# Optimization experiments

Measured on AMD Instinct MI355X. Metric: run time of the kernel, lower is better.

Reference implementation:

```python
import jax, jax.numpy as jnp
import numpy as np

D_MODEL = 1024
N_HEADS = 16
D_HEAD = 64


def setup_inputs() -> dict:
    key = jax.random.key(0)
    ks = jax.random.split(key, 9)
    B, T = 2, 2048
    s_in = 1.0 / np.sqrt(D_MODEL)
    s_o = 1.0 / np.sqrt(N_HEADS * D_HEAD)
    return {
        "x": jax.random.normal(ks[0], (B, T, D_MODEL), dtype=jnp.float32),
        "wq": jax.random.normal(ks[1], (D_MODEL, N_HEADS * D_HEAD), dtype=jnp.float32) * s_in,
        "bq": jax.random.normal(ks[2], (N_HEADS * D_HEAD,), dtype=jnp.float32) * 0.01,
        "wk": jax.random.normal(ks[3], (D_MODEL, N_HEADS * D_HEAD), dtype=jnp.float32) * s_in,
        "bk": jax.random.normal(ks[4], (N_HEADS * D_HEAD,), dtype=jnp.float32) * 0.01,
        "wv": jax.random.normal(ks[5], (D_MODEL, N_HEADS * D_HEAD), dtype=jnp.float32) * s_in,
        "bv": jax.random.normal(ks[6], (N_HEADS * D_HEAD,), dtype=jnp.float32) * 0.01,
        "wo": jax.random.normal(ks[7], (N_HEADS * D_HEAD, D_MODEL), dtype=jnp.float32) * s_o,
        "bo": jax.random.normal(ks[8], (D_MODEL,), dtype=jnp.float32) * 0.01,
    }


def reference(x, wq, bq, wk, bk, wv, bv, wo, bo):
    B, T, _ = x.shape
    H, Dh = N_HEADS, D_HEAD
    # projections -> [B, H, T, Dh]
    q = (x @ wq + bq).reshape(B, T, H, Dh).transpose(0, 2, 1, 3)
    k = (x @ wk + bk).reshape(B, T, H, Dh).transpose(0, 2, 1, 3)
    v = (x @ wv + bv).reshape(B, T, H, Dh).transpose(0, 2, 1, 3)
    scale = 1.0 / np.sqrt(Dh).astype(np.float32)
    attn = jnp.einsum("bhqd,bhkd->bhqk", q, k) * scale  # [B,H,T,T]
    causal = jnp.tril(jnp.ones((T, T), dtype=bool))
    attn = jnp.where(causal, attn, jnp.float32(-jnp.inf))
    attn = jax.nn.softmax(attn, axis=-1)
    out = jnp.einsum("bhqk,bhkd->bhqd", attn, v)  # [B,H,T,Dh]
    out = out.transpose(0, 2, 1, 3).reshape(B, T, H * Dh)
    return out @ wo + bo
```

## Files before the change

### kernel.cpp

```cpp
#include <hip/hip_runtime.h>
#include <math.h>

#define D_MODEL 1024
#define N_HEADS 16
#define D_HEAD  64
#define B_SZ    2
#define T_SEQ   2048

typedef short bf16x8 __attribute__((ext_vector_type(8)));
typedef short bf16x4 __attribute__((ext_vector_type(4)));
typedef float f32x4  __attribute__((ext_vector_type(4)));
typedef unsigned short us4 __attribute__((ext_vector_type(4)));

__device__ __forceinline__ unsigned short f2bf(float f) {
  union { float f; unsigned u; } v; v.f = f;
  unsigned r = v.u + 0x7FFFu + ((v.u >> 16) & 1u);
  return (unsigned short)(r >> 16);
}
__device__ __forceinline__ float bf2f(unsigned short s) {
  union { unsigned u; float f; } v; v.u = ((unsigned)s) << 16;
  return v.f;
}
__device__ __forceinline__ unsigned pack2_rtz(float lo, float hi) {
  union { float f; unsigned u; } a, b; a.f = hi; b.f = lo;
  return __builtin_amdgcn_perm(a.u, b.u, 0x07060302u);
}

__device__ __forceinline__ void async_copy16(const unsigned short* g, unsigned short* l) {
  __builtin_amdgcn_global_load_lds(
      (__attribute__((address_space(1))) void*)(g),
      (__attribute__((address_space(3))) void*)(l), 16, 0, 0);
}

__global__ __launch_bounds__(256) void conv_all(
    const float* __restrict__ x,
    const float* __restrict__ wq, const float* __restrict__ wk,
    const float* __restrict__ wv, const float* __restrict__ wo,
    unsigned short* __restrict__ wt, unsigned short* __restrict__ xb)
{
  const int z = blockIdx.z;
  if (z < 4) {
    const float* W = (z == 0) ? wq : (z == 1) ? wk : (z == 2) ? wv : wo;
    unsigned short* O = wt + (size_t)z * D_MODEL * D_MODEL;
    __shared__ float t[32][33];
    const int tx = threadIdx.x & 31, ty = threadIdx.x >> 5;
    const int kb = blockIdx.x * 32, nb = blockIdx.y * 32;
    #pragma unroll
    for (int i = 0; i < 4; i++)
      t[ty + i * 8][tx] = W[(size_t)(kb + ty + i * 8) * D_MODEL + nb + tx];
    __syncthreads();
    #pragma unroll
    for (int i = 0; i < 4; i++)
      O[(size_t)(nb + ty + i * 8) * D_MODEL + kb + tx] = f2bf(t[tx][ty + i * 8]);
  } else {
    const int row = (z - 4) * 1024 + blockIdx.y * 32 + (threadIdx.x >> 3);
    const int col = blockIdx.x * 32 + (threadIdx.x & 7) * 4;
    float4 v = *(const float4*)&x[(size_t)row * D_MODEL + col];
    us4 o = { f2bf(v.x), f2bf(v.y), f2bf(v.z), f2bf(v.w) };
    *(us4*)&xb[(size_t)row * D_MODEL + col] = o;
  }
}

#define BKg 64

__global__ __launch_bounds__(256) void qkv_gemm(
    const unsigned short* __restrict__ A, const unsigned short* __restrict__ Bt,
    const float* __restrict__ bq, const float* __restrict__ bk,
    const float* __restrict__ bv, unsigned short* __restrict__ qkv,
    unsigned short* __restrict__ vT)
{
  __shared__ unsigned short As[128 * BKg];
  __shared__ unsigned short Bs[64 * BKg];

  const int tid  = threadIdx.x;
  const int wv   = tid >> 6;
  const int lane = tid & 63;
  const int lr   = lane & 15;
  const int quad = lane >> 4;
  const int wm   = wv >> 1;
  const int wn   = wv & 1;
  const int row0 = blockIdx.x * 128;
  const int col0 = blockIdx.y * 64;
  const int K = D_MODEL;

  const int mid = col0 >> 10;
  const float* bias = (mid == 0) ? bq : (mid == 1) ? bk : bv;

  f32x4 acc[8];
  #pragma unroll
  for (int i = 0; i < 8; i++) acc[i] = (f32x4){0.f, 0.f, 0.f, 0.f};

  for (int k0 = 0; k0 < K; k0 += BKg) {
    #pragma unroll
    for (int it = 0; it < 4; it++) {
      const int gg = wv * 256 + it * 64 + lane;
      const int r  = gg >> 3;
      const int gc = ((gg & 7) ^ (r & 7)) * 8;
      async_copy16(A + (size_t)(row0 + r) * K + k0 + gc,
                   (unsigned short*)As + (size_t)(wv * 256 + it * 64) * 8);
    }
    #pragma unroll
    for (int it = 0; it < 2; it++) {
      const int gg = wv * 128 + it * 64 + lane;
      const int r  = gg >> 3;
      const int gc = ((gg & 7) ^ (r & 7)) * 8;
      async_copy16(Bt + (size_t)(col0 + r) * K + k0 + gc,
                   (unsigned short*)Bs + (size_t)(wv * 128 + it * 64) * 8);
    }
    __syncthreads();

    if (mid == 2) {
      bf16x8 aF[4][2], bF[2][2];
      #pragma unroll
      for (int hf = 0; hf < 2; hf++) {
        const int kc = (hf * 4 + quad) ^ (lr & 7);
        #pragma unroll
        for (int mi = 0; mi < 4; mi++)
          aF[mi][hf] = *(const bf16x8*)&As[(wm * 64 + mi * 16 + lr) * BKg + kc * 8];
        #pragma unroll
        for (int ni = 0; ni < 2; ni++)
          bF[ni][hf] = *(const bf16x8*)&Bs[(wn * 32 + ni * 16 + lr) * BKg + kc * 8];
      }
      #pragma unroll
      for (int hf = 0; hf < 2; hf++)
        #pragma unroll
        for (int mi = 0; mi < 4; mi++)
          #pragma unroll
          for (int ni = 0; ni < 2; ni++)
            acc[mi * 2 + ni] = __builtin_amdgcn_mfma_f32_16x16x32_bf16(
                aF[mi][hf], bF[ni][hf], acc[mi * 2 + ni], 0, 0, 0);
    } else {
      bf16x8 aF[2][2], bF[4][2];
      #pragma unroll
      for (int hf = 0; hf < 2; hf++) {
        const int kc = (hf * 4 + quad) ^ (lr & 7);
        #pragma unroll
        for (int mi = 0; mi < 2; mi++)
          aF[mi][hf] = *(const bf16x8*)&Bs[(wm * 32 + mi * 16 + lr) * BKg + kc * 8];
        #pragma unroll
        for (int ni = 0; ni < 4; ni++)
          bF[ni][hf] = *(const bf16x8*)&As[(wn * 64 + ni * 16 + lr) * BKg + kc * 8];
      }
      #pragma unroll
      for (int hf = 0; hf < 2; hf++)
        #pragma unroll
        for (int mi = 0; mi < 2; mi++)
          #pragma unroll
          for (int ni = 0; ni < 4; ni++)
            acc[mi * 4 + ni] = __builtin_amdgcn_mfma_f32_16x16x32_bf16(
                aF[mi][hf], bF[ni][hf], acc[mi * 4 + ni], 0, 0, 0);
    }
    __syncthreads();
  }

  if (mid == 2) {
    #pragma unroll
    for (int ni = 0; ni < 2; ni++) {
      const int nn = (col0 & 1023) + wn * 32 + ni * 16 + lr;
      const float bv_ = bias[nn];
      const int h = nn >> 6, d = nn & 63;
      #pragma unroll
      for (int mi = 0; mi < 4; mi++) {
        const int t0_ = row0 + wm * 64 + mi * 16 + quad * 4;
        const int b = t0_ >> 11, tl = t0_ & 2047;
        us4 o;
        #pragma unroll
        for (int i = 0; i < 4; i++) o[i] = f2bf(acc[mi * 2 + ni][i] + bv_);
        *(us4*)&vT[((size_t)(b * N_HEADS + h) * D_HEAD + d) * T_SEQ + tl] = o;
      }
    }
  } else {
    unsigned short* dst = qkv + (size_t)mid * (4096u * 1024u);
    #pragma unroll
    for (int ni = 0; ni < 4; ni++) {
      const int t = row0 + wn * 64 + ni * 16 + lr;
      const int b = t >> 11, tl = t & 2047;
      #pragma unroll
      for (int mi = 0; mi < 2; mi++) {
        const int f = (col0 & 1023) + wm * 32 + mi * 16 + quad * 4;
        const int h = f >> 6, d = f & 63;
        const float4 b4 = *(const float4*)&bias[f];
        us4 o;
        o[0] = f2bf(acc[mi * 4 + ni][0] + b4.x);
        o[1] = f2bf(acc[mi * 4 + ni][1] + b4.y);
        o[2] = f2bf(acc[mi * 4 + ni][2] + b4.z);
        o[3] = f2bf(acc[mi * 4 + ni][3] + b4.w);
        *(us4*)&dst[((size_t)(b * N_HEADS + h) * T_SEQ + tl) * D_HEAD + d] = o;
      }
    }
  }
}

__global__ __launch_bounds__(256) void mfma_gemm(
    const unsigned short* __restrict__ A, const unsigned short* __restrict__ Bt,
    const float* __restrict__ bias, float* __restrict__ C,
    int M, int N, int K)
{
  __shared__ unsigned short As[128 * BKg];
  __shared__ unsigned short Bs[64 * BKg];

  const int tid  = threadIdx.x;
  const int wv   = tid >> 6;
  const int lane = tid & 63;
  const int lr   = lane & 15;
  const int quad = lane >> 4;
  const int wm   = wv >> 1;
  const int wn   = wv & 1;
  const int row0 = blockIdx.x * 128;
  const int col0 = blockIdx.y * 64;

  f32x4 acc[4][2];
  #pragma unroll
  for (int mi = 0; mi < 4; mi++)
    #pragma unroll
    for (int ni = 0; ni < 2; ni++) acc[mi][ni] = (f32x4){0.f, 0.f, 0.f, 0.f};

  for (int k0 = 0; k0 < K; k0 += BKg) {
    #pragma unroll
    for (int it = 0; it < 4; it++) {
      const int gg = wv * 256 + it * 64 + lane;
      const int r  = gg >> 3;
      const int gc = ((gg & 7) ^ (r & 7)) * 8;
      async_copy16(A + (size_t)(row0 + r) * K + k0 + gc,
                   (unsigned short*)As + (size_t)(wv * 256 + it * 64) * 8);
    }
    #pragma unroll
    for (int it = 0; it < 2; it++) {
      const int gg = wv * 128 + it * 64 + lane;
      const int r  = gg >> 3;
      const int gc = ((gg & 7) ^ (r & 7)) * 8;
      async_copy16(Bt + (size_t)(col0 + r) * K + k0 + gc,
                   (unsigned short*)Bs + (size_t)(wv * 128 + it * 64) * 8);
    }
    __syncthreads();

    bf16x8 aF[4][2], bF[2][2];
    #pragma unroll
    for (int hf = 0; hf < 2; hf++) {
      const int kc = (hf * 4 + quad) ^ (lr & 7);
      #pragma unroll
      for (int mi = 0; mi < 4; mi++)
        aF[mi][hf] = *(const bf16x8*)&As[(wm * 64 + mi * 16 + lr) * BKg + kc * 8];
      #pragma unroll
      for (int ni = 0; ni < 2; ni++)
        bF[ni][hf] = *(const bf16x8*)&Bs[(wn * 32 + ni * 16 + lr) * BKg + kc * 8];
    }
    #pragma unroll
    for (int hf = 0; hf < 2; hf++)
      #pragma unroll
      for (int mi = 0; mi < 4; mi++)
        #pragma unroll
        for (int ni = 0; ni < 2; ni++)
          acc[mi][ni] = __builtin_amdgcn_mfma_f32_16x16x32_bf16(
              aF[mi][hf], bF[ni][hf], acc[mi][ni], 0, 0, 0);
    __syncthreads();
  }

  #pragma unroll
  for (int ni = 0; ni < 2; ni++) {
    const int n = col0 + wn * 32 + ni * 16 + lr;
    const float bv = bias[n];
    #pragma unroll
    for (int mi = 0; mi < 4; mi++) {
      #pragma unroll
      for (int i = 0; i < 4; i++) {
        const int m = row0 + wm * 64 + mi * 16 + quad * 4 + i;
        C[(size_t)m * N + n] = acc[mi][ni][i] + bv;
      }
    }
  }
}

__global__ __launch_bounds__(256) void flash_part(
    const unsigned short* __restrict__ Q, const unsigned short* __restrict__ K,
    const unsigned short* __restrict__ Vt, unsigned short* __restrict__ Out,
    unsigned short* __restrict__ Opart, float* __restrict__ Lpart)
{
  const int bh = blockIdx.x;
  const int y  = blockIdx.y;
  int g, md;
  if (y < 20) {
    const int k = y / 5, r = y % 5;
    if (r == 0) { g = 7 - k; md = 0; }
    else        { g = 15 - 2 * k - ((r - 1) >> 1); md = 1 + ((r - 1) & 1); }
  } else { g = 3 - (y - 20); md = 0; }

  const int b  = bh >> 4;
  const int h  = bh & 15;

  const unsigned short* Qb = Q  + (size_t)bh * T_SEQ * D_HEAD;
  const unsigned short* Kb = K  + (size_t)bh * T_SEQ * D_HEAD;
  const unsigned short* Vb = Vt + (size_t)bh * D_HEAD * T_SEQ;

  __shared__ __align__(16) unsigned short Ks[2][64 * 64];
  __shared__ __align__(16) unsigned short Vs[2][64 * 64];

  const int tid  = threadIdx.x;
  const int wv4  = tid >> 6;
  const int lane = tid & 63;
  const int lr   = lane & 15;
  const int quad = lane >> 4;

  const int qg      = 4 * g + wv4;
  const int q0      = qg * 32;
  const int my_full = 2 * g + 1 + (wv4 >> 1);
  const int tstart  = (md == 2) ? (g + 1) : 0;
  const int bend    = (md == 1) ? (g + 1) : (2 * g + 2);
  const int my_end  = (md == 1) ? (g + 1) : my_full;

  const int cbase = (tid & ~63);
  auto stage = [&](int buf, int tile) {
    const unsigned short* ksrc = Kb + (size_t)tile * 64 * D_HEAD;
    const int kv0 = tile * 64;
    #pragma unroll
    for (int it = 0; it < 2; it++) {
      const int gg = it * 256 + tid;
      const int r  = gg >> 3;
      const int gc = (gg & 7) ^ (r & 7);
      async_copy16(ksrc + r * 64 + gc * 8, &Ks[buf][(size_t)(it * 256 + cbase) * 8]);
      async_copy16(Vb + (size_t)r * T_SEQ + kv0 + gc * 8, &Vs[buf][(size_t)(it * 256 + cbase) * 8]);
    }
  };

  bf16x8 bQ[2][2];
  #pragma unroll
  for (int qb = 0; qb < 2; qb++)
    #pragma unroll
    for (int kh = 0; kh < 2; kh++)
      bQ[qb][kh] = *(const bf16x8*)&Qb[(size_t)(q0 + qb * 16 + lr) * D_HEAD + kh * 32 + quad * 8];

  f32x4 oacc[2][4];
  #pragma unroll
  for (int qb = 0; qb < 2; qb++)
    #pragma unroll
    for (int dt = 0; dt < 4; dt++) oacc[qb][dt] = (f32x4){0.f, 0.f, 0.f, 0.f};
  float l_i[2] = {0.f, 0.f};

  const float SCL2 = 0.125f * 1.44269504f;
  const float FIXM = 16.0f;

  int cur = 0;
  stage(0, tstart);

  for (int j = tstart; j < bend; j++) {
    __syncthreads();
    if (j + 1 < bend) stage(cur ^ 1, j + 1);

    if (j < my_end) {
      const unsigned short* KsB = &Ks[cur][0];
      const unsigned short* VsB = &Vs[cur][0];
      const int kv0 = j * 64;

      bf16x8 aK[4][2];
      #pragma unroll
      for (int nt = 0; nt < 4; nt++) {
        const int row = nt * 16 + lr;
        #pragma unroll
        for (int kh = 0; kh < 2; kh++) {
          const int sc = (kh * 4 + quad) ^ (row & 7);
          aK[nt][kh] = *(const bf16x8*)&KsB[row * 64 + sc * 8];
        }
      }
      bf16x4 aV[4][4];
      #pragma unroll
      for (int dt = 0; dt < 4; dt++) {
        const int row = dt * 16 + lr;
        #pragma unroll
        for (int ks = 0; ks < 4; ks++) {
          const int sc = (ks * 2 + (quad >> 1)) ^ (row & 7);
          aV[dt][ks] = *(const bf16x4*)&VsB[row * 64 + sc * 8 + (quad & 1) * 4];
        }
      }

      f32x4 sacc[2][4];
      #pragma unroll
      for (int nt = 0; nt < 4; nt++) {
        #pragma unroll
        for (int qb = 0; qb < 2; qb++) {
          f32x4 c = (f32x4){0.f, 0.f, 0.f, 0.f};
          c = __builtin_amdgcn_mfma_f32_16x16x32_bf16(aK[nt][0], bQ[qb][0], c, 0, 0, 0);
          c = __builtin_amdgcn_mfma_f32_16x16x32_bf16(aK[nt][1], bQ[qb][1], c, 0, 0, 0);
          sacc[qb][nt] = c;
        }
      }

      const bool diag = (j == my_full - 1);
      bf16x4 bP[2][4];
      #pragma unroll
      for (int qb = 0; qb < 2; qb++) {
        if (diag) {
          const int qcol = q0 + qb * 16 + lr;
          #pragma unroll
          for (int nt = 0; nt < 4; nt++)
            #pragma unroll
            for (int i = 0; i < 4; i++)
              if (kv0 + nt * 16 + quad * 4 + i > qcol) sacc[qb][nt][i] = -INFINITY;
        }
        float rs = 0.f;
        #pragma unroll
        for (int nt = 0; nt < 4; nt++) {
          float p[4];
          #pragma unroll
          for (int i = 0; i < 4; i++) {
            p[i] = __builtin_amdgcn_exp2f(fmaf(sacc[qb][nt][i], SCL2, -FIXM));
            rs += p[i];
          }
          union { unsigned u[2]; bf16x4 v; } pk;
          pk.u[0] = pack2_rtz(p[0], p[1]);
          pk.u[1] = pack2_rtz(p[2], p[3]);
          bP[qb][nt] = pk.v;
        }
        l_i[qb] += rs;
      }

      #pragma unroll
      for (int ks = 0; ks < 4; ks++)
        #pragma unroll
        for (int dt = 0; dt < 4; dt++)
          #pragma unroll
          for (int qb = 0; qb < 2; qb++)
            oacc[qb][dt] = __builtin_amdgcn_mfma_f32_16x16x16bf16_1k(
                aV[dt][ks], bP[qb][ks], oacc[qb][dt], 0, 0, 0);
    }
    cur ^= 1;
  }

  #pragma unroll
  for (int qb = 0; qb < 2; qb++) {
    l_i[qb] += __shfl_xor(l_i[qb], 16);
    l_i[qb] += __shfl_xor(l_i[qb], 32);
  }

  if (md == 0) {
    #pragma unroll
    for (int qb = 0; qb < 2; qb++) {
      const float invl = __builtin_amdgcn_rcpf(l_i[qb]);
      const size_t orow = (size_t)(b * T_SEQ + q0 + qb * 16 + lr) * D_MODEL + h * D_HEAD;
      #pragma unroll
      for (int dt = 0; dt < 4; dt++) {
        us4 o;
        #pragma unroll
        for (int i = 0; i < 4; i++) o[i] = f2bf(oacc[qb][dt][i] * invl);
        *(us4*)&Out[orow + dt * 16 + quad * 4] = o;
      }
    }
  } else {
    const int s = md - 1;
    const int p = (bh * 32 + (qg - 32)) * 2 + s;
    #pragma unroll
    for (int qb = 0; qb < 2; qb++) {
      Lpart[(p * 2 + qb) * 64 + lane] = l_i[qb];
      #pragma unroll
      for (int dt = 0; dt < 4; dt++) {
        us4 o;
        #pragma unroll
        for (int i = 0; i < 4; i++) o[i] = f2bf(oacc[qb][dt][i]);
        *(us4*)&Opart[(size_t)(((p * 8 + qb * 4 + dt) * 64) + lane) * 4] = o;
      }
    }
  }
}

__global__ __launch_bounds__(64) void flash_reduce(
    const unsigned short* __restrict__ Opart, const float* __restrict__ Lpart,
    unsigned short* __restrict__ Out)
{
  const int bh  = blockIdx.x;
  const int qgr = blockIdx.y;
  const int q0  = (32 + qgr) * 32;
  const int b   = bh >> 4;
  const int h   = bh & 15;
  const int lane = threadIdx.x;
  const int lr   = lane & 15;
  const int quad = lane >> 4;

  const int item = bh * 32 + qgr;
  const int p0 = item * 2, p1 = item * 2 + 1;

  #pragma unroll
  for (int qb = 0; qb < 2; qb++) {
    const float l0 = Lpart[(p0 * 2 + qb) * 64 + lane];
    const float l1 = Lpart[(p1 * 2 + qb) * 64 + lane];
    const float invL = __builtin_amdgcn_rcpf(l0 + l1);
    const size_t orow = (size_t)(b * T_SEQ + q0 + qb * 16 + lr) * D_MODEL + h * D_HEAD;
    #pragma unroll
    for (int dt = 0; dt < 4; dt++) {
      us4 o0 = *(const us4*)&Opart[(size_t)(((p0 * 8 + qb * 4 + dt) * 64) + lane) * 4];
      us4 o1 = *(const us4*)&Opart[(size_t)(((p1 * 8 + qb * 4 + dt) * 64) + lane) * 4];
      us4 o;
      #pragma unroll
      for (int i = 0; i < 4; i++)
        o[i] = f2bf((bf2f(o0[i]) + bf2f(o1[i])) * invL);
      *(us4*)&Out[orow + dt * 16 + quad * 4] = o;
    }
  }
}

extern "C" void kernel_launch(void* const* d_in, const int* in_sizes, int n_in,
                              void* d_out, int out_size, void* d_ws, size_t ws_size,
                              hipStream_t stream) {
  (void)in_sizes; (void)n_in; (void)out_size; (void)ws_size;

  const float* x  = (const float*)d_in[0];
  const float* wq = (const float*)d_in[1];
  const float* bq = (const float*)d_in[2];
  const float* wk = (const float*)d_in[3];
  const float* bk = (const float*)d_in[4];
  const float* wv = (const float*)d_in[5];
  const float* bv = (const float*)d_in[6];
  const float* wo = (const float*)d_in[7];
  const float* bo = (const float*)d_in[8];
  float* out = (float*)d_out;

  const int M = B_SZ * T_SEQ;
  const int N = D_MODEL;
  const int K = D_MODEL;
  const size_t MN = (size_t)M * N;
  const size_t WN = (size_t)N * N;

  unsigned short* wt    = (unsigned short*)d_ws;
  unsigned short* xb    = wt + 4 * WN;
  unsigned short* qkv   = xb + MN;
  unsigned short* qb    = qkv;
  unsigned short* kb    = qkv + MN;
  unsigned short* vT    = qkv + 2 * MN;
  unsigned short* attnb = vT + MN;
  float* Lpart = (float*)(attnb + MN);
  unsigned short* Opart = xb;

  conv_all<<<dim3(32, 32, 8), dim3(256), 0, stream>>>(x, wq, wk, wv, wo, wt, xb);

  qkv_gemm<<<dim3(M / 128, 48), dim3(256), 0, stream>>>(xb, wt, bq, bk, bv, qkv, vT);

  flash_part<<<dim3(B_SZ * N_HEADS, 24), dim3(256), 0, stream>>>(
      qb, kb, vT, attnb, Opart, Lpart);
  flash_reduce<<<dim3(B_SZ * N_HEADS, 32), dim3(64), 0, stream>>>(
      Opart, Lpart, attnb);

  mfma_gemm<<<dim3(M / 128, N / 64), dim3(256), 0, stream>>>(attnb, wt + 3 * WN, bo, out, M, N, K);
}
```

Measured before the change: 193.4 us.

## Rebalance causal flash-attention split with three-way KV partitioning via lookup table

Replaces the arithmetic block-to-work mapping with a table that splits more query groups' KV ranges, using a three-way split for the longest rows and a two-way split for mid rows, raising the grid from 24 to 32 blocks per head. The reduce kernel now combines two or three partials over 48 row groups. To make room for the larger partial buffers, the weight layout is rotated so Wo sits in slot 0 and the partials reuse the Wq slot after the QKV GEMM. This aims to even out per-block work and fill the GPU better, at the cost of more partial-result traffic and reduce work.

```diff
diff --git a/kernel.cpp b/kernel.cpp
--- a/kernel.cpp
+++ b/kernel.cpp
@@ -31,6 +31,28 @@
       (__attribute__((address_space(1))) void*)(g),
       (__attribute__((address_space(3))) void*)(l), 16, 0, 0);
 }
+
+__device__ const unsigned short FLASH_TBL[32] = {
+  (unsigned short)(11| (0<<4) | (2<<6)), (unsigned short)(11 | (1<<4) | (2<<6)),
+  (unsigned short)(15 | (0<<4) | (3<<6)), (unsigned short)(15 | (1<<4) | (3<<6)),
+  (unsigned short)(15 | (2<<4) | (3<<6)),
+  (unsigned short)(10 | (0<<4) | (2<<6)), (unsigned short)(10 | (1<<4) | (2<<6)),
+  (unsigned short)(14 | (0<<4) | (3<<6)), (unsigned short)(14 | (1<<4) | (3<<6)),
+  (unsigned short)(14 | (2<<4) | (3<<6)),
+  (unsigned short)(9  | (0<<4) | (2<<6)), (unsigned short)(9  | (1<<4) | (2<<6)),
+  (unsigned short)(13 | (0<<4) | (3<<6)), (unsigned short)(13 | (1<<4) | (3<<6)),
+  (unsigned short)(13 | (2<<4) | (3<<6)),
+  (unsigned short)(12 | (0<<4) | (3<<6)), (unsigned short)(12 | (1<<4) | (3<<6)),
+  (unsigned short)(12 | (2<<4) | (3<<6)),
+  (unsigned short)(8  | (0<<4) | (2<<6)), (unsigned short)(8  | (1<<4) | (2<<6)),
+  (unsigned short)(3  | (0<<4) | (1<<6)),
+  (unsigned short)(7  | (0<<4) | (2<<6)), (unsigned short)(7  | (1<<4) | (2<<6)),
+  (unsigned short)(6  | (0<<4) | (2<<6)), (unsigned short)(6  | (1<<4) | (2<<6)),
+  (unsigned short)(2  | (0<<4) | (1<<6)),
+  (unsigned short)(5  | (0<<4) | (2<<6)), (unsigned short)(5  | (1<<4) | (2<<6)),
+  (unsigned short)(4  | (0<<4) | (2<<6)), (unsigned short)(4  | (1<<4) | (2<<6)),
+  (unsigned short)(1  | (0<<4) | (1<<6)), (unsigned short)(0  | (0<<4) | (1<<6)),
+};
 
 __global__ __launch_bounds__(256) void conv_all(
     const float* __restrict__ x,
@@ -41,7 +63,7 @@
   const int z = blockIdx.z;
   if (z < 4) {
     const float* W = (z == 0) ? wq : (z == 1) ? wk : (z == 2) ? wv : wo;
-    unsigned short* O = wt + (size_t)z * D_MODEL * D_MODEL;
+    unsigned short* O = wt + (size_t)((z + 1) & 3) * D_MODEL * D_MODEL;
     __shared__ float t[32][33];
     const int tx = threadIdx.x & 31, ty = threadIdx.x >> 5;
     const int kb = blockIdx.x * 32, nb = blockIdx.y * 32;
@@ -277,13 +299,10 @@
     unsigned short* __restrict__ Opart, float* __restrict__ Lpart)
 {
   const int bh = blockIdx.x;
-  const int y  = blockIdx.y;
-  int g, md;
-  if (y < 20) {
-    const int k = y / 5, r = y % 5;
-    if (r == 0) { g = 7 - k; md = 0; }
-    else        { g = 15 - 2 * k - ((r - 1) >> 1); md = 1 + ((r - 1) & 1); }
-  } else { g = 3 - (y - 20); md = 0; }
+  const unsigned tv = FLASH_TBL[blockIdx.y];
+  const int g     = tv & 15;
+  const int piece = (tv >> 4) & 3;
+  const int np    = tv >> 6;
 
   const int b  = bh >> 4;
   const int h  = bh & 15;
@@ -303,10 +322,20 @@
 
   const int qg      = 4 * g + wv4;
   const int q0      = qg * 32;
-  const int my_full = 2 * g + 1 + (wv4 >> 1);
-  const int tstart  = (md == 2) ? (g + 1) : 0;
-  const int bend    = (md == 1) ? (g + 1) : (2 * g + 2);
-  const int my_end  = (md == 1) ? (g + 1) : my_full;
+  const int my_full = (qg >> 1) + 1;
+  const int ntot    = 2 * g + 2;
+
+  int lo, hi;
+  if (np == 1)      { lo = 0; hi = ntot; }
+  else if (np == 2) { lo = piece ? (g + 1) : 0; hi = piece ? ntot : (g + 1); }
+  else {
+    const int a3 = ntot / 3, b3 = (2 * ntot) / 3;
+    lo = (piece == 0) ? 0 : (piece == 1) ? a3 : b3;
+    hi = (piece == 0) ? a3 : (piece == 1) ? b3 : ntot;
+  }
+  const int tstart = lo;
+  const int bend   = hi;
+  const int my_end = (hi < my_full) ? hi : my_full;
 
   const int cbase = (tid & ~63);
   auto stage = [&](int buf, int tile) {
@@ -431,7 +460,7 @@
     l_i[qb] += __shfl_xor(l_i[qb], 32);
   }
 
-  if (md == 0) {
+  if (np == 1) {
     #pragma unroll
     for (int qb = 0; qb < 2; qb++) {
       const float invl = __builtin_amdgcn_rcpf(l_i[qb]);
@@ -445,8 +474,8 @@
       }
     }
   } else {
-    const int s = md - 1;
-    const int p = (bh * 32 + (qg - 32)) * 2 + s;
+    const int idx = (g < 12) ? ((qg - 16) * 2 + piece) : (64 + (qg - 48) * 3 + piece);
+    const int p = bh * 112 + idx;
     #pragma unroll
     for (int qb = 0; qb < 2; qb++) {
       Lpart[(p * 2 + qb) * 64 + lane] = l_i[qb];
@@ -467,30 +496,35 @@
 {
   const int bh  = blockIdx.x;
   const int qgr = blockIdx.y;
-  const int q0  = (32 + qgr) * 32;
+  const int q0  = (16 + qgr) * 32;
   const int b   = bh >> 4;
   const int h   = bh & 15;
   const int lane = threadIdx.x;
   const int lr   = lane & 15;
   const int quad = lane >> 4;
 
-  const int item = bh * 32 + qgr;
-  const int p0 = item * 2, p1 = item * 2 + 1;
+  int base, n;
+  if (qgr < 32) { base = qgr * 2;             n = 2; }
+  else          { base = 64 + (qgr - 32) * 3; n = 3; }
+  base += bh * 112;
 
   #pragma unroll
   for (int qb = 0; qb < 2; qb++) {
-    const float l0 = Lpart[(p0 * 2 + qb) * 64 + lane];
-    const float l1 = Lpart[(p1 * 2 + qb) * 64 + lane];
-    const float invL = __builtin_amdgcn_rcpf(l0 + l1);
+    float L = 0.f;
+    for (int s = 0; s < n; s++) L += Lpart[((base + s) * 2 + qb) * 64 + lane];
+    const float invL = __builtin_amdgcn_rcpf(L);
     const size_t orow = (size_t)(b * T_SEQ + q0 + qb * 16 + lr) * D_MODEL + h * D_HEAD;
     #pragma unroll
     for (int dt = 0; dt < 4; dt++) {
-      us4 o0 = *(const us4*)&Opart[(size_t)(((p0 * 8 + qb * 4 + dt) * 64) + lane) * 4];
-      us4 o1 = *(const us4*)&Opart[(size_t)(((p1 * 8 + qb * 4 + dt) * 64) + lane) * 4];
+      float acc[4] = {0.f, 0.f, 0.f, 0.f};
+      for (int s = 0; s < n; s++) {
+        us4 ov = *(const us4*)&Opart[(size_t)((((base + s) * 8 + qb * 4 + dt) * 64) + lane) * 4];
+        #pragma unroll
+        for (int i = 0; i < 4; i++) acc[i] += bf2f(ov[i]);
+      }
       us4 o;
       #pragma unroll
-      for (int i = 0; i < 4; i++)
-        o[i] = f2bf((bf2f(o0[i]) + bf2f(o1[i])) * invL);
+      for (int i = 0; i < 4; i++) o[i] = f2bf(acc[i] * invL);
       *(us4*)&Out[orow + dt * 16 + quad * 4] = o;
     }
   }
@@ -526,16 +560,16 @@
   unsigned short* vT    = qkv + 2 * MN;
   unsigned short* attnb = vT + MN;
   float* Lpart = (float*)(attnb + MN);
-  unsigned short* Opart = xb;
+  unsigned short* Opart = wt + WN;
 
   conv_all<<<dim3(32, 32, 8), dim3(256), 0, stream>>>(x, wq, wk, wv, wo, wt, xb);
 
-  qkv_gemm<<<dim3(M / 128, 48), dim3(256), 0, stream>>>(xb, wt, bq, bk, bv, qkv, vT);
-
-  flash_part<<<dim3(B_SZ * N_HEADS, 24), dim3(256), 0, stream>>>(
+  qkv_gemm<<<dim3(M / 128, 48), dim3(256), 0, stream>>>(xb, wt + WN, bq, bk, bv, qkv, vT);
+
+  flash_part<<<dim3(B_SZ * N_HEADS, 32), dim3(256), 0, stream>>>(
       qb, kb, vT, attnb, Opart, Lpart);
-  flash_reduce<<<dim3(B_SZ * N_HEADS, 32), dim3(64), 0, stream>>>(
+  flash_reduce<<<dim3(B_SZ * N_HEADS, 48), dim3(64), 0, stream>>>(
       Opart, Lpart, attnb);
 
-  mfma_gemm<<<dim3(M / 128, N / 64), dim3(256), 0, stream>>>(attnb, wt + 3 * WN, bo, out, M, N, K);
-}
+  mfma_gemm<<<dim3(M / 128, N / 64), dim3(256), 0, stream>>>(attnb, wt, bo, out, M, N, K);
+}
```

Result: slower. 204.9 us (+5.9%).
